# Kernel tuning notes

Hardware: AMD Instinct MI355X
Metric: run time of the kernel (lower is better)

Reference implementation:

```python
import jax, jax.numpy as jnp
import numpy as np

N_HEADS = 32
N_KV_HEADS = 8
HEAD_DIM = 128
HIDDEN = 4096
ROPE_BASE = 10000.0


def _rope_tables(seq_len, head_dim, base):
    inv_freq = 1.0 / (base ** (jnp.arange(0, head_dim, 2, dtype=jnp.float32) / head_dim))
    t = jnp.arange(seq_len, dtype=jnp.float32)
    freqs = jnp.outer(t, inv_freq)                    # (S, D/2)
    emb = jnp.concatenate([freqs, freqs], axis=-1)    # (S, D)
    return jnp.cos(emb), jnp.sin(emb)


def _rotate_half(x):
    half = x.shape[-1] // 2
    return jnp.concatenate([-x[..., half:], x[..., :half]], axis=-1)


def _apply_rope(x, cos, sin):
    # x: (B, H, S, D); cos/sin: (S, D)
    return x * cos[None, None] + _rotate_half(x) * sin[None, None]


def setup_inputs() -> dict:
    key = jax.random.key(0)
    k1, k2, k3 = jax.random.split(key, 3)
    bsz, q_len = 2, 2048
    total_heads = N_HEADS + 2 * N_KV_HEADS
    hidden_states = jax.random.normal(k1, (bsz, q_len, HIDDEN), dtype=jnp.float32)
    w_qkv = jax.random.normal(k2, (total_heads * HEAD_DIM, HIDDEN), dtype=jnp.float32) * 0.02
    w_o = jax.random.normal(k3, (HIDDEN, N_HEADS * HEAD_DIM), dtype=jnp.float32) * 0.02
    return {"hidden_states": hidden_states, "w_qkv": w_qkv, "w_o": w_o}


def reference(hidden_states, w_qkv, w_o):
    bsz, q_len, _ = hidden_states.shape
    n_rep = N_HEADS // N_KV_HEADS

    qkv = jnp.einsum('bsh,oh->bso', hidden_states, w_qkv)  # (B, S, total_heads*D)
    q_sz = N_HEADS * HEAD_DIM
    kv_sz = N_KV_HEADS * HEAD_DIM
    q = qkv[..., :q_sz].reshape(bsz, q_len, N_HEADS, HEAD_DIM).transpose(0, 2, 1, 3)
    k = qkv[..., q_sz:q_sz + kv_sz].reshape(bsz, q_len, N_KV_HEADS, HEAD_DIM).transpose(0, 2, 1, 3)
    v = qkv[..., q_sz + kv_sz:].reshape(bsz, q_len, N_KV_HEADS, HEAD_DIM).transpose(0, 2, 1, 3)

    cos, sin = _rope_tables(q_len, HEAD_DIM, ROPE_BASE)
    q = _apply_rope(q, cos, sin)
    k = _apply_rope(k, cos, sin)

    # repeat KV heads for GQA
    k = jnp.repeat(k, n_rep, axis=1)  # (B, H, S, D)
    v = jnp.repeat(v, n_rep, axis=1)

    scale = HEAD_DIM ** -0.5
    scores = jnp.einsum('bhqd,bhkd->bhqk', q, k) * scale
    causal = jnp.tril(jnp.ones((q_len, q_len), dtype=bool))
    scores = jnp.where(causal[None, None], scores, jnp.finfo(scores.dtype).min)
    attn = jax.nn.softmax(scores, axis=-1)
    out = jnp.einsum('bhqk,bhkd->bhqd', attn, v)  # (B, H, S, D)
    out = out.transpose(0, 2, 1, 3).reshape(bsz, q_len, N_HEADS * HEAD_DIM)
    return jnp.einsum('bso,ho->bsh', out, w_o)
```

## Files before the change

kernel.cpp:

```cpp
#include <hip/hip_runtime.h>
#include <stdint.h>

#define N_HEADS   32
#define N_KV      8
#define HEAD_DIM  128
#define HIDDEN_DIM 4096
#define BSZ       2
#define SEQ       2048
#define TOT_HEADS 48
#define QKV_DIM   6144
#define ROWS      4096
#define ROPE_HEADS 40

typedef __attribute__((ext_vector_type(4)))  float f32x4;
typedef __attribute__((ext_vector_type(16))) float f32x16;
typedef __attribute__((ext_vector_type(8)))  short bf16x8;
typedef unsigned short u16;
typedef unsigned int   u32;

#define AS1 __attribute__((address_space(1)))
#define AS3 __attribute__((address_space(3)))

static __device__ __forceinline__ float bf16f(u16 u) { return __uint_as_float(((u32)u) << 16); }
static __device__ __forceinline__ u16 f2bf(float f) {
  u32 x = __float_as_uint(f);
  x += 0x7fffu + ((x >> 16) & 1u);
  return (u16)(x >> 16);
}
static __device__ __forceinline__ u32 cvt_pk_bf16(float lo, float hi) {
  u32 r;
  asm("v_cvt_pk_bf16_f32 %0, %1, %2" : "=v"(r) : "v"(lo), "v"(hi));
  return r;
}
static __device__ __forceinline__ bf16x8 mk8(u32 a, u32 b, u32 c, u32 d) {
  union { u32 u[4]; bf16x8 v; } x;
  x.u[0] = a; x.u[1] = b; x.u[2] = c; x.u[3] = d;
  return x.v;
}

__global__ void cast3_k(const float4* __restrict__ a, const float4* __restrict__ b,
                        const float4* __restrict__ c,
                        ushort4* __restrict__ oa, ushort4* __restrict__ ob,
                        ushort4* __restrict__ oc, int na, int nb, int nc) {
  int i = blockIdx.x * blockDim.x + threadIdx.x;
  const int stride = gridDim.x * blockDim.x;
  const int tot = na + nb + nc;
  for (; i < tot; i += stride) {
    const float4* s; ushort4* d; int j = i;
    if (j < na)           { s = a; d = oa; }
    else if (j < na + nb) { s = b; d = ob; j -= na; }
    else                  { s = c; d = oc; j -= na + nb; }
    const float4 v = s[j];
    ushort4 o;
    o.x = f2bf(v.x); o.y = f2bf(v.y); o.z = f2bf(v.z); o.w = f2bf(v.w);
    d[j] = o;
  }
}

__global__ void rope_tables_k(float* __restrict__ ctab, float* __restrict__ stab) {
  int t = blockIdx.x * blockDim.x + threadIdx.x;
  if (t >= SEQ * 64) return;
  int s = t >> 6, i = t & 63;
  float inv = powf(10000.0f, -(float)i / 64.0f);
  float ang = (float)s * inv;
  float sv, cv;
  sincosf(ang, &sv, &cv);
  ctab[t] = cv; stab[t] = sv;
}

template<int F32OUT>
__global__ __launch_bounds__(256, 2)
void gemm_bt_k(const u16* __restrict__ A, const u16* __restrict__ Bw,
               void* __restrict__ C, int M, int N, int K)
{
  __shared__ uint4 smA[1024];
  __shared__ uint4 smB[1024];
  const int tid = threadIdx.x;
  const int nbx = N >> 7;
  const int bm = (blockIdx.x / nbx) << 7;
  const int bn = (blockIdx.x % nbx) << 7;
  const int lane = tid & 63;
  const int wave = tid >> 6;
  const int wm = (wave >> 1) << 6;
  const int wn = (wave & 1) << 6;
  const int fr = lane & 15;
  const int fq = lane >> 4;

  f32x4 acc[4][4];
#pragma unroll
  for (int i = 0; i < 4; ++i)
#pragma unroll
    for (int j = 0; j < 4; ++j)
      acc[i][j] = {0.f, 0.f, 0.f, 0.f};

  const int gl_r = lane >> 3;
  const int gl_c = (lane & 7) ^ gl_r;

  for (int k0 = 0; k0 < K; k0 += 64) {
#pragma unroll
    for (int i = 0; i < 4; ++i) {
      const int rbase = (wave << 5) + (i << 3);
      const int row = rbase + gl_r;
      const u16* gA = A  + (size_t)(bm + row) * K + k0 + (gl_c << 3);
      const u16* gB = Bw + (size_t)(bn + row) * K + k0 + (gl_c << 3);
      __builtin_amdgcn_global_load_lds((const AS1 u32*)gA, (AS3 u32*)&smA[rbase << 3], 16, 0, 0);
      __builtin_amdgcn_global_load_lds((const AS1 u32*)gB, (AS3 u32*)&smB[rbase << 3], 16, 0, 0);
    }
    __syncthreads();
#pragma unroll
    for (int kk = 0; kk < 2; ++kk) {
      bf16x8 af[4], bfr[4];
      const int cc = (kk << 2) + fq;
#pragma unroll
      for (int m = 0; m < 4; ++m) {
        const int row = wm + (m << 4) + fr;
        af[m] = *reinterpret_cast<const bf16x8*>(&smA[(row << 3) + (cc ^ (row & 7))]);
      }
#pragma unroll
      for (int n = 0; n < 4; ++n) {
        const int row = wn + (n << 4) + fr;
        bfr[n] = *reinterpret_cast<const bf16x8*>(&smB[(row << 3) + (cc ^ (row & 7))]);
      }
#pragma unroll
      for (int m = 0; m < 4; ++m)
#pragma unroll
        for (int n = 0; n < 4; ++n)
          acc[m][n] = __builtin_amdgcn_mfma_f32_16x16x32_bf16(af[m], bfr[n], acc[m][n], 0, 0, 0);
    }
    __syncthreads();
  }

  const int col0 = bn + wn + fr;
#pragma unroll
  for (int m = 0; m < 4; ++m) {
#pragma unroll
    for (int i = 0; i < 4; ++i) {
      const int row = bm + wm + (m << 4) + (fq << 2) + i;
      if (F32OUT) {
        float* rp = reinterpret_cast<float*>(C) + (size_t)row * N + col0;
#pragma unroll
        for (int n = 0; n < 4; ++n) rp[n << 4] = acc[m][n][i];
      } else {
        u16* rp = reinterpret_cast<u16*>(C) + (size_t)row * N + col0;
#pragma unroll
        for (int n = 0; n < 4; ++n) rp[n << 4] = f2bf(acc[m][n][i]);
      }
    }
  }
}

__global__ void rope_scatter_k(const u16* __restrict__ QKV,
                               const float* __restrict__ ctab, const float* __restrict__ stab,
                               u16* __restrict__ Qo, u16* __restrict__ Ko)
{
  const int t = blockIdx.x * blockDim.x + threadIdx.x;
  const int d = t & 63;
  const int hh = (t >> 6) % ROPE_HEADS;
  const int row = t / (64 * ROPE_HEADS);
  const int b = row >> 11, sq = row & (SEQ - 1);
  const u16* src = QKV + (size_t)row * QKV_DIM + hh * HEAD_DIM;
  const float x1 = bf16f(src[d]);
  const float x2 = bf16f(src[d + 64]);
  const float c = ctab[(sq << 6) + d], sn = stab[(sq << 6) + d];
  float y1 = x1 * c - x2 * sn;
  float y2 = x2 * c + x1 * sn;
  u16* dst;
  if (hh < N_HEADS) {
    const float SC2 = 0.1275170747f;
    y1 *= SC2; y2 *= SC2;
    dst = Qo + ((size_t)(b * N_HEADS + hh) * SEQ + sq) * HEAD_DIM;
  } else {
    dst = Ko + ((size_t)(b * N_KV + (hh - N_HEADS)) * SEQ + sq) * HEAD_DIM;
  }
  dst[d] = f2bf(y1);
  dst[d + 64] = f2bf(y2);
}

__global__ __launch_bounds__(256)
void vtrans_k(const u16* __restrict__ QKV, u16* __restrict__ Vt)
{
  __shared__ u16 tile[64][72];
  const int idx = blockIdx.x;
  const int dt = idx & 1;
  const int st = (idx >> 1) & 31;
  const int kv = (idx >> 6) & 7;
  const int b  = idx >> 9;
  const int tid = threadIdx.x;
  const int s0 = st << 6, d0 = dt << 6;
  const int rl = tid >> 3, cc8 = (tid & 7) << 3;
#pragma unroll
  for (int p = 0; p < 2; ++p) {
    const int sl = rl + (p << 5);
    const u16* src = QKV + (size_t)(b * SEQ + s0 + sl) * QKV_DIM
                   + (N_HEADS + N_KV + kv) * HEAD_DIM + d0 + cc8;
    *reinterpret_cast<uint4*>(&tile[sl][cc8]) = *reinterpret_cast<const uint4*>(src);
  }
  __syncthreads();
#pragma unroll
  for (int p = 0; p < 2; ++p) {
    const int dl = rl + (p << 5);
    u16 tmp[8];
#pragma unroll
    for (int k2 = 0; k2 < 8; ++k2) tmp[k2] = tile[cc8 + k2][dl];
    u16* dst = Vt + ((size_t)(b * N_KV + kv) * HEAD_DIM + d0 + dl) * SEQ + s0 + cc8;
    *reinterpret_cast<uint4*>(dst) = *reinterpret_cast<const uint4*>(tmp);
  }
}

__global__ __launch_bounds__(512, 2)
void attn_mfma_k(const u16* __restrict__ Q, const u16* __restrict__ K,
                 const u16* __restrict__ Vt, u16* __restrict__ Out)
{
  __shared__ uint4 Ksm[2][512];
  __shared__ uint4 Vsm[2][512];
  const int tid  = threadIdx.x;
  const int lane = tid & 63;
  const int w    = tid >> 6;
  const int idx  = blockIdx.x;
  const int kvh  = idx & 7;
  const int b    = (idx >> 3) & 1;
  const int qi   = 31 - (idx >> 4);
  const int q0   = qi << 6;
  const int head = w & 3;
  const int qsub = w >> 2;
  const int h    = (kvh << 2) + head;
  const int diag = 2 * qi + qsub;
  const int nsub = 2 * qi + 2;

  const int ql = lane & 31;
  const int hh = lane >> 5;

  const u16* Qh = Q  + (size_t)(b * N_HEADS + h) * SEQ * HEAD_DIM;
  const u16* Kb = K  + (size_t)(b * N_KV + kvh) * SEQ * HEAD_DIM;
  const u16* Vb = Vt + (size_t)(b * N_KV + kvh) * HEAD_DIM * SEQ;

  int koff[8];
#pragma unroll
  for (int f = 0; f < 8; ++f) koff[f] = (ql << 4) + (((f << 1) + hh) ^ (ql & 15));
  int voff0[4], voff1[4];
#pragma unroll
  for (int dblk = 0; dblk < 4; ++dblk) {
    const int d = (dblk << 5) + ql;
    voff0[dblk] = (d << 2) + (hh ^ (d & 3));
    voff1[dblk] = (d << 2) + ((2 + hh) ^ (d & 3));
  }

  auto stage = [&](int buf, int ks) {
    const int sl = (w << 6) + lane;
    {
      const int row = sl >> 4, cs = sl & 15;
      const int g = cs ^ (row & 15);
      const u16* src = Kb + (size_t)(ks + row) * HEAD_DIM + (g << 3);
      __builtin_amdgcn_global_load_lds((const AS1 u32*)src, (AS3 u32*)&Ksm[buf][w << 6], 16, 0, 0);
    }
    {
      const int d = sl >> 2, cs = sl & 3;
      const int g = cs ^ (d & 3);
      const u16* src = Vb + (size_t)d * SEQ + ks + (g << 3);
      __builtin_amdgcn_global_load_lds((const AS1 u32*)src, (AS3 u32*)&Vsm[buf][w << 6], 16, 0, 0);
    }
  };

  bf16x8 qf[8];
#pragma unroll
  for (int f = 0; f < 8; ++f)
    qf[f] = *reinterpret_cast<const bf16x8*>(Qh + (size_t)(q0 + (qsub << 5) + ql) * HEAD_DIM
                                             + 16 * f + 8 * hh);

  f32x16 o[4];
#pragma unroll
  for (int dblk = 0; dblk < 4; ++dblk)
#pragma unroll
    for (int r = 0; r < 16; ++r) o[dblk][r] = 0.f;
  float m2 = -1e30f, lsum = 0.f;

  stage(0, 0);

#pragma unroll 1
  for (int s = 0; s < nsub; ++s) {
    const int cur = s & 1;
    __syncthreads();
    if (s + 1 < nsub) stage(cur ^ 1, (s + 1) << 5);

    if (s <= diag) {
      f32x16 T;
#pragma unroll
      for (int r = 0; r < 16; ++r) T[r] = 0.f;
      __builtin_amdgcn_s_setprio(1);
#pragma unroll
      for (int f = 0; f < 8; ++f) {
        const bf16x8 kf = *reinterpret_cast<const bf16x8*>(&Ksm[cur][koff[f]]);
        T = __builtin_amdgcn_mfma_f32_32x32x16_bf16(kf, qf[f], T, 0, 0, 0);
      }
      __builtin_amdgcn_s_setprio(0);

      if (s == diag) {
#pragma unroll
        for (int r = 0; r < 16; ++r) {
          const int kr = (r & 3) + ((r >> 2) << 3) + (hh << 2);
          if (kr > ql) T[r] = -1e30f;
        }
      }
      float mt = T[0];
#pragma unroll
      for (int r = 1; r < 16; ++r) mt = fmaxf(mt, T[r]);
      mt = fmaxf(mt, __shfl_xor(mt, 32));

      if (__any(mt > m2 + 8.f)) {
        const float mnew = fmaxf(m2, mt);
        const float resc = exp2f(m2 - mnew);
        lsum *= resc;
#pragma unroll
        for (int r = 0; r < 16; ++r) {
          const int qr = (r & 3) + ((r >> 2) << 3) + (hh << 2);
          const float rr = __shfl(resc, qr);
#pragma unroll
          for (int dblk = 0; dblk < 4; ++dblk) o[dblk][r] *= rr;
        }
        m2 = mnew;
      }

      float ps = 0.f;
#pragma unroll
      for (int r = 0; r < 16; ++r) { const float pv = exp2f(T[r] - m2); T[r] = pv; ps += pv; }
      ps += __shfl_xor(ps, 32);
      lsum += ps;

      u32 pk[8], sw[8];
#pragma unroll
      for (int i = 0; i < 8; ++i) {
        pk[i] = cvt_pk_bf16(T[2 * i], T[2 * i + 1]);
        sw[i] = (u32)__shfl_xor((int)pk[i], 32);
      }
      const bf16x8 a0 = hh ? mk8(sw[2], sw[3], pk[2], pk[3])
                           : mk8(pk[0], pk[1], sw[0], sw[1]);
      const bf16x8 a1 = hh ? mk8(sw[6], sw[7], pk[6], pk[7])
                           : mk8(pk[4], pk[5], sw[4], sw[5]);

      __builtin_amdgcn_s_setprio(1);
#pragma unroll
      for (int dblk = 0; dblk < 4; ++dblk) {
        const bf16x8 va = *reinterpret_cast<const bf16x8*>(&Vsm[cur][voff0[dblk]]);
        o[dblk] = __builtin_amdgcn_mfma_f32_32x32x16_bf16(a0, va, o[dblk], 0, 0, 0);
        const bf16x8 vb2 = *reinterpret_cast<const bf16x8*>(&Vsm[cur][voff1[dblk]]);
        o[dblk] = __builtin_amdgcn_mfma_f32_32x32x16_bf16(a1, vb2, o[dblk], 0, 0, 0);
      }
      __builtin_amdgcn_s_setprio(0);
    }
  }

  u16* Ob = Out + (size_t)(b * SEQ + q0 + (qsub << 5)) * HIDDEN_DIM + h * HEAD_DIM + ql;
#pragma unroll
  for (int r = 0; r < 16; ++r) {
    const int qr = (r & 3) + ((r >> 2) << 3) + (hh << 2);
    const float il = 1.0f / __shfl(lsum, qr);
    u16* rp = Ob + (size_t)qr * HIDDEN_DIM;
#pragma unroll
    for (int dblk = 0; dblk < 4; ++dblk)
      rp[dblk * 32] = f2bf(o[dblk][r] * il);
  }
}

extern "C" void kernel_launch(void* const* d_in, const int* in_sizes, int n_in,
                              void* d_out, int out_size, void* d_ws, size_t ws_size,
                              hipStream_t stream)
{
  const float* hs   = (const float*)d_in[0];
  const float* wqkv = (const float*)d_in[1];
  const float* wo   = (const float*)d_in[2];
  float* out = (float*)d_out;
  char* ws = (char*)d_ws;
  size_t off = 0;
  auto alloc = [&](size_t bytes) -> void* {
    void* p = ws + off;
    off += (bytes + 255) & ~(size_t)255;
    return p;
  };
  u16* Xbf    = (u16*)alloc((size_t)ROWS * HIDDEN_DIM * 2);
  u16* Wqkvbf = (u16*)alloc((size_t)QKV_DIM * HIDDEN_DIM * 2);
  u16* Wobf   = (u16*)alloc((size_t)HIDDEN_DIM * HIDDEN_DIM * 2);
  u16* QKVbf  = (u16*)alloc((size_t)ROWS * QKV_DIM * 2);
  u16* Qbf    = (u16*)alloc((size_t)BSZ * N_HEADS * SEQ * HEAD_DIM * 2);
  u16* Kbf    = (u16*)alloc((size_t)BSZ * N_KV * SEQ * HEAD_DIM * 2);
  u16* Vtbf   = (u16*)alloc((size_t)BSZ * N_KV * SEQ * HEAD_DIM * 2);
  float* ctab = (float*)alloc((size_t)SEQ * 64 * 4);
  float* stab = (float*)alloc((size_t)SEQ * 64 * 4);
  u16* AOut   = (u16*)alloc((size_t)ROWS * HIDDEN_DIM * 2);
  if (off > ws_size) return;

  cast3_k<<<4096, 256, 0, stream>>>((const float4*)hs, (const float4*)wqkv, (const float4*)wo,
                                    (ushort4*)Xbf, (ushort4*)Wqkvbf, (ushort4*)Wobf,
                                    ROWS * HIDDEN_DIM / 4, QKV_DIM * HIDDEN_DIM / 4,
                                    HIDDEN_DIM * HIDDEN_DIM / 4);
  rope_tables_k<<<(SEQ * 64) / 256, 256, 0, stream>>>(ctab, stab);

  gemm_bt_k<0><<<(ROWS / 128) * (QKV_DIM / 128), 256, 0, stream>>>(Xbf, Wqkvbf, (void*)QKVbf,
                                                                   ROWS, QKV_DIM, HIDDEN_DIM);
  rope_scatter_k<<<ROWS * ROPE_HEADS * 64 / 256, 256, 0, stream>>>(QKVbf, ctab, stab, Qbf, Kbf);
  vtrans_k<<<BSZ * N_KV * (SEQ / 64) * (HEAD_DIM / 64), 256, 0, stream>>>(QKVbf, Vtbf);
  attn_mfma_k<<<BSZ * N_KV * (SEQ / 64), 512, 0, stream>>>(Qbf, Kbf, Vtbf, AOut);
  gemm_bt_k<1><<<(ROWS / 128) * (HIDDEN_DIM / 128), 256, 0, stream>>>(AOut, Wobf, (void*)out,
                                                                      ROWS, HIDDEN_DIM, HIDDEN_DIM);
}
```

Before: 566.0 us.

## Replace GEMM with 256x256 double-buffered pipelined kernel with XCD-aware block remap

Both projection GEMMs move from 128x128 tiles with single-buffered LDS to 256x256 tiles using 512 threads and 128KB of dynamic LDS, double-buffered across K steps. Global-to-LDS loads for later tiles are interleaved with four MFMA quadrant phases, using explicit barriers, waitcnts and setprio so memory latency overlaps compute. Block indices are remapped across the 8 XCDs to improve L2 locality. The larger tile and LDS footprint limit occupancy and produce fewer blocks (384 and 256), which may underfill the GPU's CUs.

```diff
diff --git a/kernel.cpp b/kernel.cpp
--- a/kernel.cpp
+++ b/kernel.cpp
@@ -37,6 +37,11 @@
   x.u[0] = a; x.u[1] = b; x.u[2] = c; x.u[3] = d;
   return x.v;
 }
+
+#define SBAR()  do { __builtin_amdgcn_sched_barrier(0); __builtin_amdgcn_s_barrier(); \
+                     __builtin_amdgcn_sched_barrier(0); } while (0)
+#define LGKM0() do { asm volatile("s_waitcnt lgkmcnt(0)" ::: "memory"); \
+                     __builtin_amdgcn_sched_barrier(0); } while (0)
 
 __global__ void cast3_k(const float4* __restrict__ a, const float4* __restrict__ b,
                         const float4* __restrict__ c,
@@ -69,70 +74,145 @@
 }
 
 template<int F32OUT>
-__global__ __launch_bounds__(256, 2)
-void gemm_bt_k(const u16* __restrict__ A, const u16* __restrict__ Bw,
+__global__ __launch_bounds__(512, 2)
+void gemm256_k(const u16* __restrict__ A, const u16* __restrict__ Bw,
                void* __restrict__ C, int M, int N, int K)
 {
-  __shared__ uint4 smA[1024];
-  __shared__ uint4 smB[1024];
-  const int tid = threadIdx.x;
-  const int nbx = N >> 7;
-  const int bm = (blockIdx.x / nbx) << 7;
-  const int bn = (blockIdx.x % nbx) << 7;
+  extern __shared__ uint4 lds[];
+  uint4* LA = lds;
+  uint4* LB = lds + 4096;
+  const int NT = K >> 6;
+  const int tid  = threadIdx.x;
   const int lane = tid & 63;
   const int wave = tid >> 6;
-  const int wm = (wave >> 1) << 6;
-  const int wn = (wave & 1) << 6;
+  const int nbx = N >> 8;
+  const int cpx = gridDim.x >> 3;
+  const int wg  = (blockIdx.x & 7) * cpx + (blockIdx.x >> 3);
+  const int bm = (wg / nbx) << 8;
+  const int bn = (wg % nbx) << 8;
+
+  const int wm = (wave >> 2) << 7;
+  const int wn = (wave & 3) << 6;
   const int fr = lane & 15;
   const int fq = lane >> 4;
-
-  f32x4 acc[4][4];
-#pragma unroll
-  for (int i = 0; i < 4; ++i)
-#pragma unroll
-    for (int j = 0; j < 4; ++j)
-      acc[i][j] = {0.f, 0.f, 0.f, 0.f};
-
-  const int gl_r = lane >> 3;
-  const int gl_c = (lane & 7) ^ gl_r;
-
-  for (int k0 = 0; k0 < K; k0 += 64) {
-#pragma unroll
-    for (int i = 0; i < 4; ++i) {
-      const int rbase = (wave << 5) + (i << 3);
-      const int row = rbase + gl_r;
-      const u16* gA = A  + (size_t)(bm + row) * K + k0 + (gl_c << 3);
-      const u16* gB = Bw + (size_t)(bn + row) * K + k0 + (gl_c << 3);
-      __builtin_amdgcn_global_load_lds((const AS1 u32*)gA, (AS3 u32*)&smA[rbase << 3], 16, 0, 0);
-      __builtin_amdgcn_global_load_lds((const AS1 u32*)gB, (AS3 u32*)&smB[rbase << 3], 16, 0, 0);
-    }
-    __syncthreads();
-#pragma unroll
-    for (int kk = 0; kk < 2; ++kk) {
-      bf16x8 af[4], bfr[4];
-      const int cc = (kk << 2) + fq;
-#pragma unroll
-      for (int m = 0; m < 4; ++m) {
-        const int row = wm + (m << 4) + fr;
-        af[m] = *reinterpret_cast<const bf16x8*>(&smA[(row << 3) + (cc ^ (row & 7))]);
-      }
-#pragma unroll
-      for (int n = 0; n < 4; ++n) {
-        const int row = wn + (n << 4) + fr;
-        bfr[n] = *reinterpret_cast<const bf16x8*>(&smB[(row << 3) + (cc ^ (row & 7))]);
-      }
-#pragma unroll
-      for (int m = 0; m < 4; ++m)
-#pragma unroll
-        for (int n = 0; n < 4; ++n)
-          acc[m][n] = __builtin_amdgcn_mfma_f32_16x16x32_bf16(af[m], bfr[n], acc[m][n], 0, 0, 0);
-    }
-    __syncthreads();
+  const int s7 = fr & 7;
+
+  const int rA  = (wave << 3) + (lane >> 3);
+  const int c8e = (((lane & 7) ^ (lane >> 3)) << 3);
+
+  auto SA = [&](int t, int h, int buf) {
+    uint4* d = LA + (buf << 11) + (h << 10) + (wave << 6);
+    const u16* s = A + (size_t)(bm + (h << 7) + rA) * K + (t << 6) + c8e;
+    __builtin_amdgcn_global_load_lds((const AS1 u32*)s, (AS3 u32*)d, 16, 0, 0);
+    __builtin_amdgcn_global_load_lds((const AS1 u32*)(s + (size_t)64 * K), (AS3 u32*)(d + 512), 16, 0, 0);
+  };
+  auto SB = [&](int t, int h, int buf) {
+    uint4* d = LB + (buf << 11) + (h << 10) + (wave << 6);
+    const u16* s = Bw + (size_t)(bn + (h << 7) + rA) * K + (t << 6) + c8e;
+    __builtin_amdgcn_global_load_lds((const AS1 u32*)s, (AS3 u32*)d, 16, 0, 0);
+    __builtin_amdgcn_global_load_lds((const AS1 u32*)(s + (size_t)64 * K), (AS3 u32*)(d + 512), 16, 0, 0);
+  };
+
+  f32x4 acc[8][4];
+#pragma unroll
+  for (int m = 0; m < 8; ++m)
+#pragma unroll
+    for (int n = 0; n < 4; ++n)
+      acc[m][n] = {0.f, 0.f, 0.f, 0.f};
+
+  SB(0, 0, 0); SB(0, 1, 0); SA(0, 0, 0); SA(0, 1, 0);
+  SB(1, 0, 1); SB(1, 1, 1); SA(1, 0, 1);
+  asm volatile("s_waitcnt vmcnt(6)" ::: "memory");
+  SBAR();
+
+  bf16x8 Af[4][2], B0[2][2], B1[2][2];
+
+#pragma unroll 1
+  for (int t = 0; t < NT; ++t) {
+    const int buf  = t & 1;
+    const int base = buf << 11;
+    const int abase = base + ((wm + fr) << 3);
+    const int bbase = base + ((wn + fr) << 3);
+
+#pragma unroll
+    for (int m = 0; m < 4; ++m)
+#pragma unroll
+      for (int kk = 0; kk < 2; ++kk)
+        Af[m][kk] = *reinterpret_cast<const bf16x8*>(&LA[abase + m * 128 + (((kk << 2) + fq) ^ s7)]);
+#pragma unroll
+    for (int n = 0; n < 2; ++n)
+#pragma unroll
+      for (int kk = 0; kk < 2; ++kk)
+        B0[n][kk] = *reinterpret_cast<const bf16x8*>(&LB[bbase + n * 128 + (((kk << 2) + fq) ^ s7)]);
+    if (t + 1 < NT) SA(t + 1, 1, buf ^ 1);
+    SBAR();
+    LGKM0();
+    __builtin_amdgcn_s_setprio(1);
+#pragma unroll
+    for (int m = 0; m < 4; ++m)
+#pragma unroll
+      for (int n = 0; n < 2; ++n)
+#pragma unroll
+        for (int kk = 0; kk < 2; ++kk)
+          acc[m][n] = __builtin_amdgcn_mfma_f32_16x16x32_bf16(Af[m][kk], B0[n][kk], acc[m][n], 0, 0, 0);
+    __builtin_amdgcn_s_setprio(0);
+    SBAR();
+
+#pragma unroll
+    for (int n = 0; n < 2; ++n)
+#pragma unroll
+      for (int kk = 0; kk < 2; ++kk)
+        B1[n][kk] = *reinterpret_cast<const bf16x8*>(&LB[bbase + (2 + n) * 128 + (((kk << 2) + fq) ^ s7)]);
+    SBAR();
+    LGKM0();
+    __builtin_amdgcn_s_setprio(1);
+#pragma unroll
+    for (int m = 0; m < 4; ++m)
+#pragma unroll
+      for (int n = 0; n < 2; ++n)
+#pragma unroll
+        for (int kk = 0; kk < 2; ++kk)
+          acc[m][2 + n] = __builtin_amdgcn_mfma_f32_16x16x32_bf16(Af[m][kk], B1[n][kk], acc[m][2 + n], 0, 0, 0);
+    __builtin_amdgcn_s_setprio(0);
+    SBAR();
+
+#pragma unroll
+    for (int m = 0; m < 4; ++m)
+#pragma unroll
+      for (int kk = 0; kk < 2; ++kk)
+        Af[m][kk] = *reinterpret_cast<const bf16x8*>(&LA[abase + 512 + m * 128 + (((kk << 2) + fq) ^ s7)]);
+    if (t + 2 < NT) SB(t + 2, 0, buf);
+    SBAR();
+    LGKM0();
+    __builtin_amdgcn_s_setprio(1);
+#pragma unroll
+    for (int m = 0; m < 4; ++m)
+#pragma unroll
+      for (int n = 0; n < 2; ++n)
+#pragma unroll
+        for (int kk = 0; kk < 2; ++kk)
+          acc[4 + m][2 + n] = __builtin_amdgcn_mfma_f32_16x16x32_bf16(Af[m][kk], B1[n][kk], acc[4 + m][2 + n], 0, 0, 0);
+    __builtin_amdgcn_s_setprio(0);
+    SBAR();
+
+    if (t + 2 < NT) { SB(t + 2, 1, buf); SA(t + 2, 0, buf); }
+    __builtin_amdgcn_s_setprio(1);
+#pragma unroll
+    for (int m = 0; m < 4; ++m)
+#pragma unroll
+      for (int n = 0; n < 2; ++n)
+#pragma unroll
+        for (int kk = 0; kk < 2; ++kk)
+          acc[4 + m][n] = __builtin_amdgcn_mfma_f32_16x16x32_bf16(Af[m][kk], B0[n][kk], acc[4 + m][n], 0, 0, 0);
+    __builtin_amdgcn_s_setprio(0);
+    if (t < NT - 2)       { asm volatile("s_waitcnt vmcnt(6)" ::: "memory"); }
+    else if (t == NT - 2) { asm volatile("s_waitcnt vmcnt(0)" ::: "memory"); }
+    SBAR();
   }
 
   const int col0 = bn + wn + fr;
 #pragma unroll
-  for (int m = 0; m < 4; ++m) {
+  for (int m = 0; m < 8; ++m) {
 #pragma unroll
     for (int i = 0; i < 4; ++i) {
       const int row = bm + wm + (m << 4) + (fq << 2) + i;
@@ -388,17 +468,22 @@
   u16* AOut   = (u16*)alloc((size_t)ROWS * HIDDEN_DIM * 2);
   if (off > ws_size) return;
 
+  (void)hipFuncSetAttribute(reinterpret_cast<const void*>(&gemm256_k<0>),
+                            hipFuncAttributeMaxDynamicSharedMemorySize, 131072);
+  (void)hipFuncSetAttribute(reinterpret_cast<const void*>(&gemm256_k<1>),
+                            hipFuncAttributeMaxDynamicSharedMemorySize, 131072);
+
   cast3_k<<<4096, 256, 0, stream>>>((const float4*)hs, (const float4*)wqkv, (const float4*)wo,
                                     (ushort4*)Xbf, (ushort4*)Wqkvbf, (ushort4*)Wobf,
                                     ROWS * HIDDEN_DIM / 4, QKV_DIM * HIDDEN_DIM / 4,
                                     HIDDEN_DIM * HIDDEN_DIM / 4);
   rope_tables_k<<<(SEQ * 64) / 256, 256, 0, stream>>>(ctab, stab);
 
-  gemm_bt_k<0><<<(ROWS / 128) * (QKV_DIM / 128), 256, 0, stream>>>(Xbf, Wqkvbf, (void*)QKVbf,
-                                                                   ROWS, QKV_DIM, HIDDEN_DIM);
+  gemm256_k<0><<<(ROWS / 256) * (QKV_DIM / 256), 512, 131072, stream>>>(Xbf, Wqkvbf, (void*)QKVbf,
+                                                                        ROWS, QKV_DIM, HIDDEN_DIM);
   rope_scatter_k<<<ROWS * ROPE_HEADS * 64 / 256, 256, 0, stream>>>(QKVbf, ctab, stab, Qbf, Kbf);
   vtrans_k<<<BSZ * N_KV * (SEQ / 64) * (HEAD_DIM / 64), 256, 0, stream>>>(QKVbf, Vtbf);
   attn_mfma_k<<<BSZ * N_KV * (SEQ / 64), 512, 0, stream>>>(Qbf, Kbf, Vtbf, AOut);
-  gemm_bt_k<1><<<(ROWS / 128) * (HIDDEN_DIM / 128), 256, 0, stream>>>(AOut, Wobf, (void*)out,
-                                                                      ROWS, HIDDEN_DIM, HIDDEN_DIM);
-}
+  gemm256_k<1><<<(ROWS / 256) * (HIDDEN_DIM / 256), 512, 131072, stream>>>(AOut, Wobf, (void*)out,
+                                                                           ROWS, HIDDEN_DIM, HIDDEN_DIM);
+}
```

After: 545.6 us. 3.6% less time.
